# Kernel tuning notes

Hardware: AMD Instinct MI355X
Metric: run time of the kernel (lower is better)

## Reference

```python
import jax, jax.numpy as jnp
import numpy as np

BATCH, SRC_LEN, DIM = 64, 2048, 1024


def setup_inputs() -> dict:
    key = jax.random.key(0)
    ks = jax.random.split(key, 8)
    s = 1.0 / np.sqrt(DIM)
    return {
        "source": jax.random.normal(ks[0], (BATCH, DIM), jnp.float32),
        "memory_bank": jax.random.normal(ks[1], (BATCH, SRC_LEN, DIM), jnp.float32),
        "condition": jax.random.normal(ks[2], (BATCH, DIM), jnp.float32),
        "W_query": jax.random.uniform(ks[3], (DIM, DIM), jnp.float32, -s, s),
        "b_query": jax.random.uniform(ks[4], (DIM,), jnp.float32, -s, s),
        "W_context": jax.random.uniform(ks[5], (DIM, DIM), jnp.float32, -s, s),
        "W_condition": jax.random.uniform(ks[6], (DIM, DIM), jnp.float32, -s, s),
        "v": jax.random.uniform(ks[7], (DIM,), jnp.float32, -s, s),
    }


def reference(source, memory_bank, condition, W_query, b_query, W_context, W_condition, v):
    # Bahdanau MLP score: v^T tanh(W_q q + U_a h_j + W_c cond)
    wq = source @ W_query.T + b_query                      # [b, d]
    wcond = condition @ W_condition.T                      # [b, d]
    uh = jnp.einsum('bsd,ed->bse', memory_bank, W_context) # [b, s, d]
    wquh = jnp.tanh(uh + (wq + wcond)[:, None, :])         # [b, s, d]
    align = jnp.einsum('bsd,d->bs', wquh, v)               # [b, s]
    align_vectors = jax.nn.softmax(align, axis=-1)         # [b, s]
    c = jnp.einsum('bs,bsd->bd', align_vectors, memory_bank)  # [b, d]
    return c, align_vectors[:, None, :]
```

## Files before the change

### kernel.cpp

```cpp
#include <hip/hip_runtime.h>

#define NBATCH 64
#define SRCLEN 2048
#define DIMK 1024
#define MROWS (NBATCH * SRCLEN)
#define NNB 4

typedef __attribute__((ext_vector_type(4))) float f32x4;
typedef __attribute__((ext_vector_type(8))) short bf16x8;

#define AS_GLOBAL __attribute__((address_space(1)))
#define AS_LDS __attribute__((address_space(3)))

__device__ __forceinline__ int cvt_pk_bf16(float a, float b) {
#if __has_builtin(__builtin_amdgcn_cvt_pk_bf16_f32)
  auto p = __builtin_amdgcn_cvt_pk_bf16_f32(a, b);
  return __builtin_bit_cast(int, p);
#else
  unsigned ua = __float_as_uint(a), ub = __float_as_uint(b);
  ua = (ua + 0x7fffu + ((ua >> 16) & 1u)) >> 16;
  ub = (ub + 0x7fffu + ((ub >> 16) & 1u)) & 0xffff0000u;
  return (int)(ua | ub);
#endif
}

__device__ __forceinline__ float fast_tanh(float x) {
#if __has_builtin(__builtin_amdgcn_exp2f) && __has_builtin(__builtin_amdgcn_rcpf)
  float e = __builtin_amdgcn_exp2f(x * 2.885390081777927f);
  return 1.0f - 2.0f * __builtin_amdgcn_rcpf(e + 1.0f);
#else
  float cx = fminf(15.f, fmaxf(-15.f, x));
  float e = __expf(2.0f * cx);
  return (e - 1.0f) / (e + 1.0f);
#endif
}

__global__ __launch_bounds__(256) void cvt_wc_kernel(const float* __restrict__ W,
                                                     unsigned short* __restrict__ Wb) {
  int i = (blockIdx.x * 256 + threadIdx.x) * 4;
  f32x4 x = *(const f32x4*)(W + i);
  int2 o;
  o.x = cvt_pk_bf16(x[0], x[1]);
  o.y = cvt_pk_bf16(x[2], x[3]);
  *(int2*)(Wb + i) = o;
}

__global__ __launch_bounds__(256) void bias_kernel(
    const float* __restrict__ src, const float* __restrict__ cond,
    const float* __restrict__ Wq, const float* __restrict__ bq,
    const float* __restrict__ Wcd, float* __restrict__ biasOut) {
  const int b = blockIdx.y, nb = blockIdx.x, tid = threadIdx.x;
  const int w = tid >> 6, lane = tid & 63;
  __shared__ float sl[1024], cl[1024];
  *(f32x4*)(sl + (tid << 2)) = *(const f32x4*)(src + (b << 10) + (tid << 2));
  *(f32x4*)(cl + (tid << 2)) = *(const f32x4*)(cond + (b << 10) + (tid << 2));
  __syncthreads();
  f32x4 s4[4], c4[4];
#pragma unroll
  for (int u = 0; u < 4; ++u) {
    s4[u] = *(const f32x4*)(sl + (lane << 4) + (u << 2));
    c4[u] = *(const f32x4*)(cl + (lane << 4) + (u << 2));
  }
  for (int it = 0; it < 32; ++it) {
    const int n = (nb << 7) + (w << 5) + it;
    const float* wq = Wq + (size_t)n * DIMK + (lane << 4);
    const float* wc = Wcd + (size_t)n * DIMK + (lane << 4);
    float a = 0.f;
#pragma unroll
    for (int u = 0; u < 4; ++u) {
      f32x4 q4 = *(const f32x4*)(wq + (u << 2));
      f32x4 w4 = *(const f32x4*)(wc + (u << 2));
      a += q4[0] * s4[u][0] + q4[1] * s4[u][1] + q4[2] * s4[u][2] + q4[3] * s4[u][3];
      a += w4[0] * c4[u][0] + w4[1] * c4[u][1] + w4[2] * c4[u][2] + w4[3] * c4[u][3];
    }
#pragma unroll
    for (int xm = 1; xm < 64; xm <<= 1) a += __shfl_xor(a, xm, 64);
    if (lane == 0) biasOut[(b << 10) + n] = a + bq[n];
  }
}

__global__ __launch_bounds__(256, 2) void gemm_align_kernel(
    const float* __restrict__ mb, const unsigned short* __restrict__ Wc,
    const float* __restrict__ bias, const float* __restrict__ v,
    float* __restrict__ alignP) {
  __shared__ float As[128 * 64];
  __shared__ unsigned short Bs[256 * 64];
  __shared__ float red[2][128];

  const int tid = threadIdx.x;
  const int lane = tid & 63;
  const int w = tid >> 6;
  const int wm = w & 1, wn = w >> 1;
  const int lr = lane & 15, quad = lane >> 4;
  const int nb = blockIdx.x;
  const int m0 = blockIdx.y << 7;
  const int n0 = nb << 8;

  f32x4 acc[4][8] = {};

  for (int kt = 0; kt < 16; ++kt) {
#pragma unroll
    for (int r = 0; r < 8; ++r) {
      int q = (w << 3) + r;
      int row = (q << 2) + (lane >> 4);
      int c = (lane & 15) ^ (row & 15);
      const float* g = mb + (size_t)(m0 + row) * DIMK + (kt << 6) + (c << 2);
      __builtin_amdgcn_global_load_lds((const AS_GLOBAL unsigned*)g,
                                       (AS_LDS unsigned*)(As + q * 256), 16, 0, 0);
    }
#pragma unroll
    for (int r = 0; r < 8; ++r) {
      int q = (w << 3) + r;
      int row = (q << 3) + (lane >> 3);
      int c = (lane & 7) ^ (lane >> 3);
      const unsigned short* g = Wc + (size_t)(n0 + row) * DIMK + (kt << 6) + (c << 3);
      __builtin_amdgcn_global_load_lds((const AS_GLOBAL unsigned*)g,
                                       (AS_LDS unsigned*)(Bs + q * 512), 16, 0, 0);
    }
    __syncthreads();

#pragma unroll
    for (int ks = 0; ks < 2; ++ks) {
      bf16x8 af[4];
#pragma unroll
      for (int i = 0; i < 4; ++i) {
        int row = (wm << 6) + (i << 4) + lr;
        int p0 = ((ks << 3) + (quad << 1)) ^ lr;
        f32x4 lo = *(const f32x4*)(As + (row << 6) + (p0 << 2));
        f32x4 hi = *(const f32x4*)(As + (row << 6) + ((p0 ^ 1) << 2));
        union { int i4[4]; bf16x8 v8; } u;
        u.i4[0] = cvt_pk_bf16(lo[0], lo[1]);
        u.i4[1] = cvt_pk_bf16(lo[2], lo[3]);
        u.i4[2] = cvt_pk_bf16(hi[0], hi[1]);
        u.i4[3] = cvt_pk_bf16(hi[2], hi[3]);
        af[i] = u.v8;
      }
#pragma unroll
      for (int j = 0; j < 8; ++j) {
        int row = (wn << 7) + (j << 4) + lr;
        int pb = ((ks << 2) + quad) ^ (lr & 7);
        bf16x8 bf = *(const bf16x8*)(Bs + (row << 6) + (pb << 3));
#pragma unroll
        for (int i = 0; i < 4; ++i)
          acc[i][j] = __builtin_amdgcn_mfma_f32_16x16x32_bf16(af[i], bf, acc[i][j], 0, 0, 0);
      }
    }
    __syncthreads();
  }

  const int b = m0 >> 11;
  float rowsum[4][4] = {};
#pragma unroll
  for (int j = 0; j < 8; ++j) {
    int n = n0 + (wn << 7) + (j << 4) + lr;
    float bn = bias[(b << 10) + n];
    float vn = v[n];
#pragma unroll
    for (int i = 0; i < 4; ++i)
#pragma unroll
      for (int rg = 0; rg < 4; ++rg) {
        float t = fast_tanh(acc[i][j][rg] + bn);
        rowsum[i][rg] = fmaf(t, vn, rowsum[i][rg]);
      }
  }
#pragma unroll
  for (int xm = 1; xm < 16; xm <<= 1)
#pragma unroll
    for (int i = 0; i < 4; ++i)
#pragma unroll
      for (int rg = 0; rg < 4; ++rg)
        rowsum[i][rg] += __shfl_xor(rowsum[i][rg], xm, 64);
  if (lr == 0) {
#pragma unroll
    for (int i = 0; i < 4; ++i)
#pragma unroll
      for (int rg = 0; rg < 4; ++rg)
        red[wn][(wm << 6) + (i << 4) + (quad << 2) + rg] = rowsum[i][rg];
  }
  __syncthreads();
  if (tid < 128)
    alignP[(size_t)nb * MROWS + m0 + tid] = red[0][tid] + red[1][tid];
}

__global__ __launch_bounds__(256) void softmax_kernel(const float* __restrict__ alignP,
                                                      float* __restrict__ outA) {
  const int b = blockIdx.x, tid = threadIdx.x;
  float loc[8];
  float mx = -3.0e38f;
#pragma unroll
  for (int r = 0; r < 8; ++r) {
    int s = (r << 8) + tid;
    float a = 0.f;
#pragma unroll
    for (int q = 0; q < NNB; ++q) a += alignP[(size_t)q * MROWS + (b << 11) + s];
    loc[r] = a;
    mx = fmaxf(mx, a);
  }
#pragma unroll
  for (int o = 32; o > 0; o >>= 1) mx = fmaxf(mx, __shfl_xor(mx, o, 64));
  __shared__ float sred[8];
  if ((tid & 63) == 0) sred[tid >> 6] = mx;
  __syncthreads();
  mx = fmaxf(fmaxf(sred[0], sred[1]), fmaxf(sred[2], sred[3]));
  float sum = 0.f;
#pragma unroll
  for (int r = 0; r < 8; ++r) {
    loc[r] = __expf(loc[r] - mx);
    sum += loc[r];
  }
#pragma unroll
  for (int o = 32; o > 0; o >>= 1) sum += __shfl_xor(sum, o, 64);
  __syncthreads();
  if ((tid & 63) == 0) sred[4 + (tid >> 6)] = sum;
  __syncthreads();
  sum = sred[4] + sred[5] + sred[6] + sred[7];
  float inv = 1.0f / sum;
#pragma unroll
  for (int r = 0; r < 8; ++r) outA[(b << 11) + (r << 8) + tid] = loc[r] * inv;
}

__global__ __launch_bounds__(256) void ctx_partial_kernel(const float* __restrict__ mb,
                                                          const float* __restrict__ wgt,
                                                          float* __restrict__ cP) {
  const int chunk = blockIdx.x, b = blockIdx.y, tid = threadIdx.x;
  __shared__ float wl[64];
  if (tid < 64) wl[tid] = wgt[(b << 11) + (chunk << 6) + tid];
  __syncthreads();
  const float* base = mb + ((size_t)(b << 11) + (chunk << 6)) * DIMK + (tid << 2);
  f32x4 a = {0.f, 0.f, 0.f, 0.f};
#pragma unroll 4
  for (int s = 0; s < 64; ++s) {
    f32x4 m4 = *(const f32x4*)(base + (size_t)s * DIMK);
    a += m4 * wl[s];
  }
  *(f32x4*)(cP + ((size_t)((chunk << 6) + b) << 10) + (tid << 2)) = a;
}

__global__ __launch_bounds__(256) void ctx_reduce_kernel(const float* __restrict__ cP,
                                                         float* __restrict__ out) {
  int idx = blockIdx.x * 256 + threadIdx.x;
  float s = 0.f;
#pragma unroll
  for (int c = 0; c < 32; ++c) s += cP[(size_t)(c << 16) + idx];
  out[idx] = s;
}

extern "C" void kernel_launch(void* const* d_in, const int* in_sizes, int n_in,
                              void* d_out, int out_size, void* d_ws, size_t ws_size,
                              hipStream_t stream) {
  const float* source = (const float*)d_in[0];
  const float* mb = (const float*)d_in[1];
  const float* cond = (const float*)d_in[2];
  const float* Wq = (const float*)d_in[3];
  const float* bq = (const float*)d_in[4];
  const float* Wc = (const float*)d_in[5];
  const float* Wcd = (const float*)d_in[6];
  const float* v = (const float*)d_in[7];
  float* out = (float*)d_out;

  char* ws = (char*)d_ws;
  unsigned short* Wc_bf = (unsigned short*)ws;
  float* bias = (float*)(ws + (2u << 20));
  float* alignP = (float*)(ws + (2u << 20) + (256u << 10));
  float* cP = (float*)(ws + (4u << 20) + (256u << 10));

  cvt_wc_kernel<<<1024, 256, 0, stream>>>(Wc, Wc_bf);
  bias_kernel<<<dim3(8, 64), 256, 0, stream>>>(source, cond, Wq, bq, Wcd, bias);
  gemm_align_kernel<<<dim3(NNB, 1024), 256, 0, stream>>>(mb, Wc_bf, bias, v, alignP);
  softmax_kernel<<<64, 256, 0, stream>>>(alignP, out + NBATCH * DIMK);
  ctx_partial_kernel<<<dim3(32, 64), 256, 0, stream>>>(mb, out + NBATCH * DIMK, cP);
  ctx_reduce_kernel<<<256, 256, 0, stream>>>(cP, out);
}
```

Measured before the change: 1.145 ms.

## Restructure align GEMM: 512-thread blocks, bf16 A staging, smaller K tiles

The Bahdanau score GEMM moves to 512-thread blocks with eight waves, each computing a 64x64 sub-tile, and halves the K tile to 32. The fp32 memory-bank tile now goes through registers and is converted to bf16 once before the LDS store, rather than being held as fp32 in LDS and converted on every fragment read. This halves A-tile LDS use, removes repeated conversions and allows higher occupancy. In exchange there are twice as many K iterations, each with two barriers. The next tile's Wc prefetch into LDS is also issued before the first barrier with no trailing barrier, so a fast wave may overwrite Bs while slower waves still read it. The partial align scores are stored transposed so softmax can sum them with one vector load, and the context loop unroll is raised.

```diff
diff --git a/kernel.cpp b/kernel.cpp
--- a/kernel.cpp
+++ b/kernel.cpp
@@ -79,13 +79,13 @@
   }
 }
 
-__global__ __launch_bounds__(256, 2) void gemm_align_kernel(
+__global__ __launch_bounds__(512, 4) void gemm_align_kernel(
     const float* __restrict__ mb, const unsigned short* __restrict__ Wc,
     const float* __restrict__ bias, const float* __restrict__ v,
-    float* __restrict__ alignP) {
-  __shared__ float As[128 * 64];
-  __shared__ unsigned short Bs[256 * 64];
-  __shared__ float red[2][128];
+    float* __restrict__ alignPt) {
+  __shared__ unsigned short As[128 * 32];
+  __shared__ unsigned short Bs[256 * 32];
+  __shared__ float red[4][128];
 
   const int tid = threadIdx.x;
   const int lane = tid & 63;
@@ -96,63 +96,59 @@
   const int m0 = blockIdx.y << 7;
   const int n0 = nb << 8;
 
-  f32x4 acc[4][8] = {};
-
-  for (int kt = 0; kt < 16; ++kt) {
-#pragma unroll
-    for (int r = 0; r < 8; ++r) {
-      int q = (w << 3) + r;
-      int row = (q << 2) + (lane >> 4);
-      int c = (lane & 15) ^ (row & 15);
-      const float* g = mb + (size_t)(m0 + row) * DIMK + (kt << 6) + (c << 2);
-      __builtin_amdgcn_global_load_lds((const AS_GLOBAL unsigned*)g,
-                                       (AS_LDS unsigned*)(As + q * 256), 16, 0, 0);
+  const int arow = tid >> 3;
+  const int acol = (tid & 7) << 2;
+  const float* gA = mb + (size_t)(m0 + arow) * DIMK + acol;
+  const int ap = (((tid & 7) >> 1) ^ ((tid >> 4) & 3));
+  unsigned short* aw0 = As + (arow << 5) + (ap << 3) + ((tid & 1) << 2);
+  unsigned short* aw1 = aw0 + (64 << 5);
+
+  const int brow0 = (w << 5) + (lane >> 2);
+  const int bc = ((lane & 3) ^ ((lane >> 3) & 3));
+  const unsigned short* gB0 = Wc + (size_t)(n0 + brow0) * DIMK + (bc << 3);
+  const unsigned short* gB1 = gB0 + (size_t)16 * DIMK;
+
+  const int fsw = (quad ^ ((lr >> 1) & 3)) << 3;
+  const unsigned short* ard = As + (((wm << 6) + lr) << 5) + fsw;
+  const unsigned short* brd = Bs + (((wn << 6) + lr) << 5) + fsw;
+
+  f32x4 acc[4][4] = {};
+
+  for (int kt = 0; kt < 32; ++kt) {
+    const int ko = kt << 5;
+    f32x4 xa0 = *(const f32x4*)(gA + ko);
+    f32x4 xa1 = *(const f32x4*)(gA + (64 * DIMK) + ko);
+    __builtin_amdgcn_global_load_lds((const AS_GLOBAL unsigned*)(gB0 + ko),
+                                     (AS_LDS unsigned*)(Bs + (w << 10)), 16, 0, 0);
+    __builtin_amdgcn_global_load_lds((const AS_GLOBAL unsigned*)(gB1 + ko),
+                                     (AS_LDS unsigned*)(Bs + (w << 10) + 512), 16, 0, 0);
+    __syncthreads();
+    int2 o0, o1;
+    o0.x = cvt_pk_bf16(xa0[0], xa0[1]);
+    o0.y = cvt_pk_bf16(xa0[2], xa0[3]);
+    o1.x = cvt_pk_bf16(xa1[0], xa1[1]);
+    o1.y = cvt_pk_bf16(xa1[2], xa1[3]);
+    *(int2*)aw0 = o0;
+    *(int2*)aw1 = o1;
+    __syncthreads();
+
+    bf16x8 af[4];
+#pragma unroll
+    for (int i = 0; i < 4; ++i) af[i] = *(const bf16x8*)(ard + (i << 9));
+#pragma unroll
+    for (int j = 0; j < 4; ++j) {
+      bf16x8 bf = *(const bf16x8*)(brd + (j << 9));
+#pragma unroll
+      for (int i = 0; i < 4; ++i)
+        acc[i][j] = __builtin_amdgcn_mfma_f32_16x16x32_bf16(af[i], bf, acc[i][j], 0, 0, 0);
     }
-#pragma unroll
-    for (int r = 0; r < 8; ++r) {
-      int q = (w << 3) + r;
-      int row = (q << 3) + (lane >> 3);
-      int c = (lane & 7) ^ (lane >> 3);
-      const unsigned short* g = Wc + (size_t)(n0 + row) * DIMK + (kt << 6) + (c << 3);
-      __builtin_amdgcn_global_load_lds((const AS_GLOBAL unsigned*)g,
-                                       (AS_LDS unsigned*)(Bs + q * 512), 16, 0, 0);
-    }
-    __syncthreads();
-
-#pragma unroll
-    for (int ks = 0; ks < 2; ++ks) {
-      bf16x8 af[4];
-#pragma unroll
-      for (int i = 0; i < 4; ++i) {
-        int row = (wm << 6) + (i << 4) + lr;
-        int p0 = ((ks << 3) + (quad << 1)) ^ lr;
-        f32x4 lo = *(const f32x4*)(As + (row << 6) + (p0 << 2));
-        f32x4 hi = *(const f32x4*)(As + (row << 6) + ((p0 ^ 1) << 2));
-        union { int i4[4]; bf16x8 v8; } u;
-        u.i4[0] = cvt_pk_bf16(lo[0], lo[1]);
-        u.i4[1] = cvt_pk_bf16(lo[2], lo[3]);
-        u.i4[2] = cvt_pk_bf16(hi[0], hi[1]);
-        u.i4[3] = cvt_pk_bf16(hi[2], hi[3]);
-        af[i] = u.v8;
-      }
-#pragma unroll
-      for (int j = 0; j < 8; ++j) {
-        int row = (wn << 7) + (j << 4) + lr;
-        int pb = ((ks << 2) + quad) ^ (lr & 7);
-        bf16x8 bf = *(const bf16x8*)(Bs + (row << 6) + (pb << 3));
-#pragma unroll
-        for (int i = 0; i < 4; ++i)
-          acc[i][j] = __builtin_amdgcn_mfma_f32_16x16x32_bf16(af[i], bf, acc[i][j], 0, 0, 0);
-      }
-    }
-    __syncthreads();
   }
 
   const int b = m0 >> 11;
   float rowsum[4][4] = {};
 #pragma unroll
-  for (int j = 0; j < 8; ++j) {
-    int n = n0 + (wn << 7) + (j << 4) + lr;
+  for (int j = 0; j < 4; ++j) {
+    int n = n0 + (wn << 6) + (j << 4) + lr;
     float bn = bias[(b << 10) + n];
     float vn = v[n];
 #pragma unroll
@@ -179,10 +175,11 @@
   }
   __syncthreads();
   if (tid < 128)
-    alignP[(size_t)nb * MROWS + m0 + tid] = red[0][tid] + red[1][tid];
-}
-
-__global__ __launch_bounds__(256) void softmax_kernel(const float* __restrict__ alignP,
+    alignPt[(size_t)(m0 + tid) * NNB + nb] =
+        red[0][tid] + red[1][tid] + red[2][tid] + red[3][tid];
+}
+
+__global__ __launch_bounds__(256) void softmax_kernel(const float* __restrict__ alignPt,
                                                       float* __restrict__ outA) {
   const int b = blockIdx.x, tid = threadIdx.x;
   float loc[8];
@@ -190,9 +187,8 @@
 #pragma unroll
   for (int r = 0; r < 8; ++r) {
     int s = (r << 8) + tid;
-    float a = 0.f;
-#pragma unroll
-    for (int q = 0; q < NNB; ++q) a += alignP[(size_t)q * MROWS + (b << 11) + s];
+    f32x4 p = *(const f32x4*)(alignPt + (size_t)((b << 11) + s) * NNB);
+    float a = p[0] + p[1] + p[2] + p[3];
     loc[r] = a;
     mx = fmaxf(mx, a);
   }
@@ -228,7 +224,7 @@
   __syncthreads();
   const float* base = mb + ((size_t)(b << 11) + (chunk << 6)) * DIMK + (tid << 2);
   f32x4 a = {0.f, 0.f, 0.f, 0.f};
-#pragma unroll 4
+#pragma unroll 8
   for (int s = 0; s < 64; ++s) {
     f32x4 m4 = *(const f32x4*)(base + (size_t)s * DIMK);
     a += m4 * wl[s];
@@ -261,13 +257,13 @@
   char* ws = (char*)d_ws;
   unsigned short* Wc_bf = (unsigned short*)ws;
   float* bias = (float*)(ws + (2u << 20));
-  float* alignP = (float*)(ws + (2u << 20) + (256u << 10));
+  float* alignPt = (float*)(ws + (2u << 20) + (256u << 10));
   float* cP = (float*)(ws + (4u << 20) + (256u << 10));
 
   cvt_wc_kernel<<<1024, 256, 0, stream>>>(Wc, Wc_bf);
   bias_kernel<<<dim3(8, 64), 256, 0, stream>>>(source, cond, Wq, bq, Wcd, bias);
-  gemm_align_kernel<<<dim3(NNB, 1024), 256, 0, stream>>>(mb, Wc_bf, bias, v, alignP);
-  softmax_kernel<<<64, 256, 0, stream>>>(alignP, out + NBATCH * DIMK);
+  gemm_align_kernel<<<dim3(NNB, 1024), 512, 0, stream>>>(mb, Wc_bf, bias, v, alignPt);
+  softmax_kernel<<<64, 256, 0, stream>>>(alignPt, out + NBATCH * DIMK);
   ctx_partial_kernel<<<dim3(32, 64), 256, 0, stream>>>(mb, out + NBATCH * DIMK, cP);
   ctx_reduce_kernel<<<256, 256, 0, stream>>>(cP, out);
 }
```

Result: slower. 1.192 ms (+4.1%).
